# Kernel tuning notes

Hardware: AMD Instinct MI355X
Metric: run time of the kernel (lower is better)

## Reference

```python
import jax, jax.numpy as jnp
import numpy as np

B, T, C, NH = 32, 784, 384, 6
HD = C // NH
SCALE = float(C) ** -0.5  # source uses dim_out**-0.5, not per-head
BN_EPS = 1e-5


def _dw_bn(xs, cw, g, b, m, v, h, w):
    # xs: [B, T, C] tokens -> depthwise 3x3 conv + eval-mode BN -> [B, T, C]
    Bn, Tn, Cn = xs.shape
    img = xs.transpose(0, 2, 1).reshape(Bn, Cn, h, w)  # b (h w) c -> b c h w
    y = jax.lax.conv_general_dilated(
        img, cw, window_strides=(1, 1), padding=((1, 1), (1, 1)),
        dimension_numbers=("NCHW", "OIHW", "NCHW"), feature_group_count=Cn)
    inv = g / jnp.sqrt(v + BN_EPS)
    y = y * inv[None, :, None, None] + (b - m * inv)[None, :, None, None]
    return y.reshape(Bn, Cn, h * w).transpose(0, 2, 1)  # b c h w -> b (h w) c


def setup_inputs() -> dict:
    key = jax.random.key(0)
    ks = jax.random.split(key, 9)
    d = {"x": jax.random.normal(ks[0], (B, T, C), jnp.float32), "h": 28, "w": 28}
    for i, nm in enumerate(["q", "k", "v"]):
        d[f"conv_w_{nm}"] = jax.random.normal(ks[1 + i], (C, 1, 3, 3), jnp.float32) * 0.2
        d[f"gamma_{nm}"] = jnp.ones((C,), jnp.float32)
        d[f"beta_{nm}"] = jnp.zeros((C,), jnp.float32)
        d[f"mean_{nm}"] = jnp.zeros((C,), jnp.float32)
        d[f"var_{nm}"] = jnp.ones((C,), jnp.float32)
    d["w_q"] = jax.random.normal(ks[4], (C, C), jnp.float32) * 0.02
    d["w_k"] = jax.random.normal(ks[5], (C, C), jnp.float32) * 0.02
    d["w_v"] = jax.random.normal(ks[6], (C, C), jnp.float32) * 0.02
    d["w_proj"] = jax.random.normal(ks[7], (C, C), jnp.float32) * 0.02
    d["b_proj"] = jnp.zeros((C,), jnp.float32)
    return d


def reference(x, h, w,
              conv_w_q, gamma_q, beta_q, mean_q, var_q,
              conv_w_k, gamma_k, beta_k, mean_k, var_k,
              conv_w_v, gamma_v, beta_v, mean_v, var_v,
              w_q, w_k, w_v, w_proj, b_proj):
    qt = _dw_bn(x, conv_w_q, gamma_q, beta_q, mean_q, var_q, h, w)
    kt = _dw_bn(x, conv_w_k, gamma_k, beta_k, mean_k, var_k, h, w)
    vt = _dw_bn(x, conv_w_v, gamma_v, beta_v, mean_v, var_v, h, w)
    Bn, Tn, Cn = x.shape
    # torch Linear: y = x @ W.T; split heads: b t (h d) -> b h t d
    q = (qt @ w_q.T).reshape(Bn, Tn, NH, HD).transpose(0, 2, 1, 3)
    k = (kt @ w_k.T).reshape(Bn, Tn, NH, HD).transpose(0, 2, 1, 3)
    v = (vt @ w_v.T).reshape(Bn, Tn, NH, HD).transpose(0, 2, 1, 3)
    attn = jnp.einsum("bhld,bhtd->bhlt", q, k) * SCALE
    attn = jax.nn.softmax(attn, axis=-1)
    o = jnp.einsum("bhlt,bhtd->bhld", attn, v)
    o = o.transpose(0, 2, 1, 3).reshape(Bn, Tn, Cn)  # b h t d -> b t (h d)
    return o @ w_proj.T + b_proj
```

## Files before the change

kernel.cpp:

```cpp
#include <hip/hip_runtime.h>

typedef __attribute__((ext_vector_type(8))) short bhalf8;
typedef __attribute__((ext_vector_type(4))) float floatx4;

#define MFMA16 __builtin_amdgcn_mfma_f32_16x16x32_bf16
#define SCALE_EXP2 0.07362225f

__device__ __forceinline__ unsigned short f2bf(float f) {
  union { float fl; unsigned u; } v;
  v.fl = f;
  unsigned r = v.u + 0x7fffu + ((v.u >> 16) & 1u);
  return (unsigned short)(r >> 16);
}
__device__ __forceinline__ unsigned fbits(float f) {
  union { float fl; unsigned u; } v; v.fl = f; return v.u;
}

typedef const __attribute__((address_space(1))) unsigned int* gas1_t;
typedef __attribute__((address_space(3))) unsigned int* las3_t;
__device__ __forceinline__ void async16(const void* g, void* l) {
  __builtin_amdgcn_global_load_lds((gas1_t)g, (las3_t)l, 16, 0, 0);
}

struct __align__(8) us4 { unsigned short x, y, z, w; };

__global__ __launch_bounds__(256) void cvtw_prep_kernel(
    const float* __restrict__ wq, const float* __restrict__ wk,
    const float* __restrict__ wv, const float* __restrict__ wp,
    unsigned short* __restrict__ o,
    const float* __restrict__ cwq, const float* __restrict__ gq,
    const float* __restrict__ bq,  const float* __restrict__ mq,
    const float* __restrict__ vq,
    const float* __restrict__ cwk, const float* __restrict__ gk,
    const float* __restrict__ bk,  const float* __restrict__ mk,
    const float* __restrict__ vk,
    const float* __restrict__ cwv, const float* __restrict__ gv,
    const float* __restrict__ bv,  const float* __restrict__ mv,
    const float* __restrict__ vv,
    float* __restrict__ fx) {
  if (blockIdx.x < 576) {
    int i = blockIdx.x * 256 + threadIdx.x;
    o[i]          = f2bf(wq[i]);
    o[147456 + i] = f2bf(wk[i]);
    o[294912 + i] = f2bf(wv[i]);
    o[442368 + i] = f2bf(wp[i]);
    return;
  }
  const float* cw[3] = {cwq, cwk, cwv};
  const float* gg[3] = {gq, gk, gv};
  const float* bb[3] = {bq, bk, bv};
  const float* mm[3] = {mq, mk, mv};
  const float* vr[3] = {vq, vk, vv};
  for (int c = threadIdx.x; c < 384; c += 256) {
#pragma unroll
    for (int cv = 0; cv < 3; ++cv) {
#pragma unroll
      for (int i = 0; i < 9; ++i) fx[cv * 3456 + i * 384 + c] = cw[cv][c * 9 + i];
      float inv = gg[cv][c] * rsqrtf(vr[cv][c] + 1e-5f);
      fx[10368 + cv * 768 + c]       = inv;
      fx[10368 + cv * 768 + 384 + c] = bb[cv][c] - mm[cv][c] * inv;
    }
  }
}

__global__ __launch_bounds__(384) void dwconv_bn_kernel(
    const float* __restrict__ x, const float* __restrict__ fx,
    unsigned short* __restrict__ qt, unsigned short* __restrict__ kt,
    unsigned short* __restrict__ vt) {
  __shared__ __align__(16) float4 Wl[3168];
  const int tid = threadIdx.x;
  for (int i = tid; i < 3168; i += 384) Wl[i] = ((const float4*)fx)[i];
  const int tok = tid / 96;
  const int g   = tid - tok * 96;
  int blk = blockIdx.x;
  int b   = blk / 98;
  int rr  = blk - b * 98;
  int yp  = rr / 7;
  int xg  = rr - yp * 7;
  int y0  = yp * 2;
  int xx  = xg * 4 + tok;
  const float4* xv = (const float4*)x;
  float4 z4 = {0.f, 0.f, 0.f, 0.f};
  float4 tap[4][3];
#pragma unroll
  for (int dy = 0; dy < 4; ++dy)
#pragma unroll
    for (int dx = 0; dx < 3; ++dx) {
      int yy = y0 - 1 + dy, xc = xx - 1 + dx;
      bool ok = ((unsigned)yy < 28u) & ((unsigned)xc < 28u);
      tap[dy][dx] = ok ? xv[((size_t)b * 784 + yy * 28 + xc) * 96 + g] : z4;
    }
  __syncthreads();
  unsigned short* outs[3] = {qt, kt, vt};
  size_t o0 = ((size_t)b * 784 + y0 * 28 + xx) * 96 + g;
#pragma unroll
  for (int cv = 0; cv < 3; ++cv) {
    float4 s0 = z4, s1 = z4;
#pragma unroll
    for (int i = 0; i < 9; ++i) {
      int dy = i / 3, dx = i - dy * 3;
      float4 w = Wl[cv * 864 + i * 96 + g];
      float4 a = tap[dy][dx];
      float4 c = tap[dy + 1][dx];
      s0.x += a.x * w.x; s0.y += a.y * w.y; s0.z += a.z * w.z; s0.w += a.w * w.w;
      s1.x += c.x * w.x; s1.y += c.y * w.y; s1.z += c.z * w.z; s1.w += c.w * w.w;
    }
    float4 inv = Wl[2592 + cv * 192 + g];
    float4 sh  = Wl[2592 + cv * 192 + 96 + g];
    us4 o;
    o.x = f2bf(s0.x * inv.x + sh.x);
    o.y = f2bf(s0.y * inv.y + sh.y);
    o.z = f2bf(s0.z * inv.z + sh.z);
    o.w = f2bf(s0.w * inv.w + sh.w);
    ((us4*)outs[cv])[o0] = o;
    o.x = f2bf(s1.x * inv.x + sh.x);
    o.y = f2bf(s1.y * inv.y + sh.y);
    o.z = f2bf(s1.z * inv.z + sh.z);
    o.w = f2bf(s1.w * inv.w + sh.w);
    ((us4*)outs[cv])[o0 + 28 * 96] = o;
  }
}

__global__ __launch_bounds__(256) void gemm128_kernel(
    const unsigned short* __restrict__ A0, const unsigned short* __restrict__ A1,
    const unsigned short* __restrict__ A2, const unsigned short* __restrict__ wbf,
    const float* __restrict__ bias,
    unsigned short* __restrict__ qh, unsigned short* __restrict__ kh,
    unsigned short* __restrict__ vht, float* __restrict__ dout, int mode) {
  __shared__ __align__(16) unsigned short SB[17408];
  unsigned short* Al = SB;
  unsigned short* Bl = SB + 8192;
  const unsigned short* A;
  const unsigned short* W;
  int epi;
  float osc = 1.f;
  unsigned short* outb = nullptr;
  if (mode == 0) {
    int z = blockIdx.z;
    A = (z == 0) ? A0 : ((z == 1) ? A1 : A2);
    W = wbf + z * 147456;
    epi = (z == 2) ? 1 : 0;
    outb = (z == 0) ? qh : ((z == 1) ? kh : vht);
    if (z == 0) osc = SCALE_EXP2;
  } else {
    A = A0; W = wbf + 442368; epi = 2;
  }
  const int nb = blockIdx.x * 128, mb = blockIdx.y * 128;
  const int tid = threadIdx.x, lane = tid & 63;
  const int wid = tid >> 6;
  const int wr = wid >> 1, wc = wid & 1;
  const int quad = lane >> 4, l15 = lane & 15;
  floatx4 zf = {0.f, 0.f, 0.f, 0.f};
  floatx4 acc[4][4] = {{zf, zf, zf, zf}, {zf, zf, zf, zf},
                       {zf, zf, zf, zf}, {zf, zf, zf, zf}};
  for (int k0 = 0; k0 < 384; k0 += 64) {
#pragma unroll
    for (int i = 0; i < 4; ++i) {
      int chunk = tid + i * 256;
      int r = chunk >> 3, c8 = chunk & 7;
      int kcol = k0 + ((c8 ^ (r & 7)) * 8);
      async16(&A[(size_t)(mb + r) * 384 + kcol], &Al[((tid & 192) + i * 256) * 8]);
      async16(&W[(size_t)(nb + r) * 384 + kcol], &Bl[((tid & 192) + i * 256) * 8]);
    }
    __syncthreads();
    bhalf8 af[4][2], bf[4][2];
#pragma unroll
    for (int mi = 0; mi < 4; ++mi)
#pragma unroll
      for (int s = 0; s < 2; ++s) {
        int row = wr * 64 + mi * 16 + l15;
        af[mi][s] = *(const bhalf8*)&Al[row * 64 + (((s * 4 + quad) ^ (row & 7)) * 8)];
        int col = wc * 64 + mi * 16 + l15;
        bf[mi][s] = *(const bhalf8*)&Bl[col * 64 + (((s * 4 + quad) ^ (col & 7)) * 8)];
      }
#pragma unroll
    for (int mi = 0; mi < 4; ++mi)
#pragma unroll
      for (int ni = 0; ni < 4; ++ni) {
        acc[mi][ni] = MFMA16(af[mi][0], bf[ni][0], acc[mi][ni], 0, 0, 0);
        acc[mi][ni] = MFMA16(af[mi][1], bf[ni][1], acc[mi][ni], 0, 0, 0);
      }
    __syncthreads();
  }
  if (epi == 2) {
#pragma unroll
    for (int mi = 0; mi < 4; ++mi)
#pragma unroll
      for (int ni = 0; ni < 4; ++ni)
#pragma unroll
        for (int r = 0; r < 4; ++r) {
          int m = mb + wr * 64 + mi * 16 + quad * 4 + r;
          int n = nb + wc * 64 + ni * 16 + l15;
          dout[(size_t)m * 384 + n] = acc[mi][ni][r] + bias[n];
        }
  } else if (epi == 0) {
#pragma unroll
    for (int mi = 0; mi < 4; ++mi)
#pragma unroll
      for (int ni = 0; ni < 4; ++ni)
#pragma unroll
        for (int r = 0; r < 4; ++r) {
          int m = mb + wr * 64 + mi * 16 + quad * 4 + r;
          int n = nb + wc * 64 + ni * 16 + l15;
          int b = m / 784, t = m - b * 784;
          outb[(((size_t)b * 6 + (n >> 6)) * 784 + t) * 64 + (n & 63)] =
              f2bf(acc[mi][ni][r] * osc);
        }
  } else {
#pragma unroll
    for (int mi = 0; mi < 4; ++mi)
#pragma unroll
      for (int ni = 0; ni < 4; ++ni) {
        int nl = wc * 64 + ni * 16 + l15;
        int ml = wr * 64 + mi * 16 + quad * 4;
        unsigned lo = ((unsigned)f2bf(acc[mi][ni][1]) << 16) | f2bf(acc[mi][ni][0]);
        unsigned hi = ((unsigned)f2bf(acc[mi][ni][3]) << 16) | f2bf(acc[mi][ni][2]);
        uint2 pk = {lo, hi};
        *(uint2*)&SB[nl * 136 + ml] = pk;
      }
    __syncthreads();
#pragma unroll
    for (int p = 0; p < 8; ++p) {
      int idx = tid + p * 256;
      int row = idx >> 4, ck = idx & 15;
      int m0 = mb + ck * 8;
      int b = m0 / 784, t0 = m0 - b * 784;
      bhalf8 vv = *(const bhalf8*)&SB[row * 136 + ck * 8];
      *(bhalf8*)&vht[(size_t)b * 301056 + (size_t)(nb + row) * 784 + t0] = vv;
    }
  }
}

__global__ __launch_bounds__(256, 4) void attn_kernel(
    const unsigned short* __restrict__ Q, const unsigned short* __restrict__ K,
    const unsigned short* __restrict__ Vt, unsigned short* __restrict__ O) {
  __shared__ __align__(16) unsigned short Kl[2][64 * 64];
  __shared__ __align__(16) unsigned short Vl[2][64 * 64];
  const int bh = blockIdx.x, qb = blockIdx.y * 128;
  const int tid = threadIdx.x, lane = tid & 63, wid = tid >> 6;
  const int quad = lane >> 4, l15 = lane & 15;
  const size_t hb = (size_t)bh * 50176;
  const unsigned short* Qh = Q + hb;
  const unsigned short* Kh = K + hb;
  const unsigned short* Vh = Vt + hb;

  auto stage = [&](int kb2, int bufS) {
#pragma unroll
    for (int i = 0; i < 2; ++i) {
      int c = tid + i * 256;
      int tt = c >> 3, c8 = c & 7;
      int sw = (c8 ^ (tt & 7)) * 8;
      int row = kb2 + tt; if (row > 783) row = 783;
      async16(&Kh[(size_t)row * 64 + sw], &Kl[bufS][((tid & 192) + i * 256) * 8]);
      int col = kb2 + sw; if (col > 776) col = 776;
      async16(&Vh[(size_t)tt * 784 + col], &Vl[bufS][((tid & 192) + i * 256) * 8]);
    }
  };

  bhalf8 zs = {0, 0, 0, 0, 0, 0, 0, 0};
  bhalf8 aq[2][2];
#pragma unroll
  for (int nt = 0; nt < 2; ++nt) {
    int row = qb + wid * 32 + nt * 16 + l15;
#pragma unroll
    for (int d = 0; d < 2; ++d)
      aq[nt][d] = (row < 784) ? *(const bhalf8*)&Qh[(size_t)row * 64 + d * 32 + quad * 8]
                              : zs;
  }

  const int addrA = (((quad & 1) * 32) + l15) * 4;
  const int addrB = addrA + 64;
  const bhalf8 ones = {16256, 16256, 16256, 16256, 16256, 16256, 16256, 16256};

  floatx4 zf = {0.f, 0.f, 0.f, 0.f};
  floatx4 accO[2][4] = {{zf, zf, zf, zf}, {zf, zf, zf, zf}};
  floatx4 accl[2] = {zf, zf};

  stage(0, 0);
  __syncthreads();

  for (int kt = 0; kt < 13; ++kt) {
    const int buf = kt & 1;
    const int kb = kt * 64;
    if (kt < 12) stage(kb + 64, buf ^ 1);

#pragma unroll
    for (int s = 0; s < 2; ++s) {
      if (kb + s * 32 >= 784) break;
      const bool tok1 = (kb + s * 32 + 16) < 784;
      bhalf8 kk[2][2], vvs[4];
#pragma unroll
      for (int h = 0; h < 2; ++h)
#pragma unroll
        for (int d = 0; d < 2; ++d) {
          int tr = (2 * s + h) * 16 + l15;
          kk[h][d] = *(const bhalf8*)&Kl[buf][tr * 64 + (((d * 4 + quad) ^ (tr & 7)) * 8)];
        }
#pragma unroll
      for (int dt = 0; dt < 4; ++dt) {
        int dr = dt * 16 + l15;
        vvs[dt] = *(const bhalf8*)&Vl[buf][dr * 64 + (((s * 4 + quad) ^ (dr & 7)) * 8)];
      }
#pragma unroll
      for (int nt = 0; nt < 2; ++nt) {
        uint2 pk0 = {0u, 0u}, pk1 = {0u, 0u};
        {
          floatx4 sf = zf;
          sf = MFMA16(kk[0][0], aq[nt][0], sf, 0, 0, 0);
          sf = MFMA16(kk[0][1], aq[nt][1], sf, 0, 0, 0);
          pk0.x = __builtin_amdgcn_perm(fbits(exp2f(sf[1])), fbits(exp2f(sf[0])),
                                        0x07060302u);
          pk0.y = __builtin_amdgcn_perm(fbits(exp2f(sf[3])), fbits(exp2f(sf[2])),
                                        0x07060302u);
        }
        if (tok1) {
          floatx4 sf = zf;
          sf = MFMA16(kk[1][0], aq[nt][0], sf, 0, 0, 0);
          sf = MFMA16(kk[1][1], aq[nt][1], sf, 0, 0, 0);
          pk1.x = __builtin_amdgcn_perm(fbits(exp2f(sf[1])), fbits(exp2f(sf[0])),
                                        0x07060302u);
          pk1.y = __builtin_amdgcn_perm(fbits(exp2f(sf[3])), fbits(exp2f(sf[2])),
                                        0x07060302u);
        }
        unsigned wa0 = __builtin_amdgcn_ds_bpermute(addrA, (int)pk0.x);
        unsigned wa1 = __builtin_amdgcn_ds_bpermute(addrA, (int)pk0.y);
        unsigned wa2 = __builtin_amdgcn_ds_bpermute(addrB, (int)pk0.x);
        unsigned wa3 = __builtin_amdgcn_ds_bpermute(addrB, (int)pk0.y);
        unsigned wb0 = 0u, wb1 = 0u, wb2 = 0u, wb3 = 0u;
        if (tok1) {
          wb0 = __builtin_amdgcn_ds_bpermute(addrA, (int)pk1.x);
          wb1 = __builtin_amdgcn_ds_bpermute(addrA, (int)pk1.y);
          wb2 = __builtin_amdgcn_ds_bpermute(addrB, (int)pk1.x);
          wb3 = __builtin_amdgcn_ds_bpermute(addrB, (int)pk1.y);
        }
        const bool hi = (quad & 2);
        union { uint4 u; bhalf8 v; } pf;
        pf.u.x = hi ? wb0 : wa0;
        pf.u.y = hi ? wb1 : wa1;
        pf.u.z = hi ? wb2 : wa2;
        pf.u.w = hi ? wb3 : wa3;
        accl[nt] = MFMA16(ones, pf.v, accl[nt], 0, 0, 0);
#pragma unroll
        for (int dt = 0; dt < 4; ++dt)
          accO[nt][dt] = MFMA16(vvs[dt], pf.v, accO[nt][dt], 0, 0, 0);
      }
    }
    __syncthreads();
  }

  const int b = bh / 6, h = bh - b * 6;
#pragma unroll
  for (int nt = 0; nt < 2; ++nt) {
    float iv = 1.f / accl[nt][0];
    int q = qb + wid * 32 + nt * 16 + l15;
    if (q < 784) {
#pragma unroll
      for (int dt = 0; dt < 4; ++dt) {
        us4 o;
        o.x = f2bf(accO[nt][dt][0] * iv);
        o.y = f2bf(accO[nt][dt][1] * iv);
        o.z = f2bf(accO[nt][dt][2] * iv);
        o.w = f2bf(accO[nt][dt][3] * iv);
        *(us4*)&O[((size_t)b * 784 + q) * 384 + h * 64 + dt * 16 + quad * 4] = o;
      }
    }
  }
}

extern "C" void kernel_launch(void* const* d_in, const int* in_sizes, int n_in,
                              void* d_out, int out_size, void* d_ws, size_t ws_size,
                              hipStream_t stream) {
  const float* x   = (const float*)d_in[0];
  const float* cwq = (const float*)d_in[3];
  const float* gq  = (const float*)d_in[4];
  const float* bq  = (const float*)d_in[5];
  const float* mq  = (const float*)d_in[6];
  const float* vq  = (const float*)d_in[7];
  const float* cwk = (const float*)d_in[8];
  const float* gk  = (const float*)d_in[9];
  const float* bk  = (const float*)d_in[10];
  const float* mk  = (const float*)d_in[11];
  const float* vk  = (const float*)d_in[12];
  const float* cwv = (const float*)d_in[13];
  const float* gv  = (const float*)d_in[14];
  const float* bv  = (const float*)d_in[15];
  const float* mv  = (const float*)d_in[16];
  const float* vv  = (const float*)d_in[17];
  const float* wq  = (const float*)d_in[18];
  const float* wk  = (const float*)d_in[19];
  const float* wv  = (const float*)d_in[20];
  const float* wp  = (const float*)d_in[21];
  const float* bp  = (const float*)d_in[22];

  unsigned short* ws = (unsigned short*)d_ws;
  const size_t SZ = (size_t)25088 * 384;
  unsigned short* qt  = ws;
  unsigned short* ktt = ws + SZ;
  unsigned short* vtt = ws + 2 * SZ;
  unsigned short* qh  = ws + 3 * SZ;
  unsigned short* kh  = ws + 4 * SZ;
  unsigned short* vht = ws + 5 * SZ;
  unsigned short* wbf = ws + 6 * SZ;
  float* fx = (float*)(ws + 5 * SZ);
  unsigned short* ob = qt;

  cvtw_prep_kernel<<<dim3(577), dim3(256), 0, stream>>>(
      wq, wk, wv, wp, wbf,
      cwq, gq, bq, mq, vq, cwk, gk, bk, mk, vk, cwv, gv, bv, mv, vv, fx);
  dwconv_bn_kernel<<<dim3(3136), dim3(384), 0, stream>>>(x, fx, qt, ktt, vtt);
  gemm128_kernel<<<dim3(3, 196, 3), dim3(256), 0, stream>>>(
      qt, ktt, vtt, wbf, bp, qh, kh, vht, (float*)d_out, 0);
  attn_kernel<<<dim3(192, 7), dim3(256), 0, stream>>>(qh, kh, vht, ob);
  gemm128_kernel<<<dim3(3, 196, 1), dim3(256), 0, stream>>>(
      ob, ktt, vtt, wbf, bp, qh, kh, vht, (float*)d_out, 1);
}
```

Measured before the change: 297.6 us.

## Remap GEMM blocks per XCD, use permlane swaps and skip padded query warps

The projection GEMM now remaps workgroup IDs so that consecutive tiles land on the same XCD, which is meant to improve L2 reuse of shared A/W rows. In the attention kernel, the ds_bpermute-based fragment shuffle is replaced by permlane32/permlane16 swap instructions, which avoids LDS-crossbar traffic. exp2f becomes the raw hardware exp2 builtin, and warps whose query rows fall entirely past 784 now skip their compute. These changes trade exactness of exp2 at extreme inputs and rely on the swap lane ordering matching the old layout.

```diff
diff --git a/kernel.cpp b/kernel.cpp
--- a/kernel.cpp
+++ b/kernel.cpp
@@ -145,7 +145,15 @@
   } else {
     A = A0; W = wbf + 442368; epi = 2;
   }
-  const int nb = blockIdx.x * 128, mb = blockIdx.y * 128;
+  const int nwg  = gridDim.x * gridDim.y;
+  const int orig = blockIdx.y * gridDim.x + blockIdx.x;
+  const int qq = nwg >> 3, rr8 = nwg & 7;
+  const int sft = (int)((unsigned)(blockIdx.z * nwg) & 7u);
+  const int xcd = (orig + sft) & 7;
+  int base = 0;
+  for (int c = 0; c < xcd; ++c) base += qq + ((((c - sft) & 7) < rr8) ? 1 : 0);
+  const int nid = base + (orig >> 3);
+  const int nb = (nid % gridDim.x) * 128, mb = (nid / gridDim.x) * 128;
   const int tid = threadIdx.x, lane = tid & 63;
   const int wid = tid >> 6;
   const int wr = wid >> 1, wc = wid & 1;
@@ -257,19 +265,21 @@
     }
   };
 
+  const int row0 = qb + wid * 32;
+  const bool w0v = row0 < 784;
+  const bool w1v = (row0 + 16) < 784;
+
   bhalf8 zs = {0, 0, 0, 0, 0, 0, 0, 0};
   bhalf8 aq[2][2];
 #pragma unroll
   for (int nt = 0; nt < 2; ++nt) {
-    int row = qb + wid * 32 + nt * 16 + l15;
+    int row = row0 + nt * 16 + l15;
 #pragma unroll
     for (int d = 0; d < 2; ++d)
       aq[nt][d] = (row < 784) ? *(const bhalf8*)&Qh[(size_t)row * 64 + d * 32 + quad * 8]
                               : zs;
   }
 
-  const int addrA = (((quad & 1) * 32) + l15) * 4;
-  const int addrB = addrA + 64;
   const bhalf8 ones = {16256, 16256, 16256, 16256, 16256, 16256, 16256, 16256};
 
   floatx4 zf = {0.f, 0.f, 0.f, 0.f};
@@ -287,6 +297,7 @@
 #pragma unroll
     for (int s = 0; s < 2; ++s) {
       if (kb + s * 32 >= 784) break;
+      if (!w0v) continue;
       const bool tok1 = (kb + s * 32 + 16) < 784;
       bhalf8 kk[2][2], vvs[4];
 #pragma unroll
@@ -303,42 +314,39 @@
       }
 #pragma unroll
       for (int nt = 0; nt < 2; ++nt) {
+        if (nt == 1 && !w1v) break;
         uint2 pk0 = {0u, 0u}, pk1 = {0u, 0u};
         {
           floatx4 sf = zf;
           sf = MFMA16(kk[0][0], aq[nt][0], sf, 0, 0, 0);
           sf = MFMA16(kk[0][1], aq[nt][1], sf, 0, 0, 0);
-          pk0.x = __builtin_amdgcn_perm(fbits(exp2f(sf[1])), fbits(exp2f(sf[0])),
+          pk0.x = __builtin_amdgcn_perm(fbits(__builtin_amdgcn_exp2f(sf[1])),
+                                        fbits(__builtin_amdgcn_exp2f(sf[0])),
                                         0x07060302u);
-          pk0.y = __builtin_amdgcn_perm(fbits(exp2f(sf[3])), fbits(exp2f(sf[2])),
+          pk0.y = __builtin_amdgcn_perm(fbits(__builtin_amdgcn_exp2f(sf[3])),
+                                        fbits(__builtin_amdgcn_exp2f(sf[2])),
                                         0x07060302u);
         }
         if (tok1) {
           floatx4 sf = zf;
           sf = MFMA16(kk[1][0], aq[nt][0], sf, 0, 0, 0);
           sf = MFMA16(kk[1][1], aq[nt][1], sf, 0, 0, 0);
-          pk1.x = __builtin_amdgcn_perm(fbits(exp2f(sf[1])), fbits(exp2f(sf[0])),
+          pk1.x = __builtin_amdgcn_perm(fbits(__builtin_amdgcn_exp2f(sf[1])),
+                                        fbits(__builtin_amdgcn_exp2f(sf[0])),
                                         0x07060302u);
-          pk1.y = __builtin_amdgcn_perm(fbits(exp2f(sf[3])), fbits(exp2f(sf[2])),
+          pk1.y = __builtin_amdgcn_perm(fbits(__builtin_amdgcn_exp2f(sf[3])),
+                                        fbits(__builtin_amdgcn_exp2f(sf[2])),
                                         0x07060302u);
         }
-        unsigned wa0 = __builtin_amdgcn_ds_bpermute(addrA, (int)pk0.x);
-        unsigned wa1 = __builtin_amdgcn_ds_bpermute(addrA, (int)pk0.y);
-        unsigned wa2 = __builtin_amdgcn_ds_bpermute(addrB, (int)pk0.x);
-        unsigned wa3 = __builtin_amdgcn_ds_bpermute(addrB, (int)pk0.y);
-        unsigned wb0 = 0u, wb1 = 0u, wb2 = 0u, wb3 = 0u;
-        if (tok1) {
-          wb0 = __builtin_amdgcn_ds_bpermute(addrA, (int)pk1.x);
-          wb1 = __builtin_amdgcn_ds_bpermute(addrA, (int)pk1.y);
-          wb2 = __builtin_amdgcn_ds_bpermute(addrB, (int)pk1.x);
-          wb3 = __builtin_amdgcn_ds_bpermute(addrB, (int)pk1.y);
-        }
-        const bool hi = (quad & 2);
+        auto sw0 = __builtin_amdgcn_permlane32_swap((int)pk0.x, (int)pk1.x, false, false);
+        auto sw1 = __builtin_amdgcn_permlane32_swap((int)pk0.y, (int)pk1.y, false, false);
+        auto f0 = __builtin_amdgcn_permlane16_swap(sw0[0], sw0[1], false, false);
+        auto f1 = __builtin_amdgcn_permlane16_swap(sw1[0], sw1[1], false, false);
         union { uint4 u; bhalf8 v; } pf;
-        pf.u.x = hi ? wb0 : wa0;
-        pf.u.y = hi ? wb1 : wa1;
-        pf.u.z = hi ? wb2 : wa2;
-        pf.u.w = hi ? wb3 : wa3;
+        pf.u.x = (unsigned)f0[0];
+        pf.u.y = (unsigned)f1[0];
+        pf.u.z = (unsigned)f0[1];
+        pf.u.w = (unsigned)f1[1];
         accl[nt] = MFMA16(ones, pf.v, accl[nt], 0, 0, 0);
 #pragma unroll
         for (int dt = 0; dt < 4; ++dt)
```

After: 263.6 us. -11.4%, faster.
